# Kernel optimization log

Hardware: AMD Instinct MI355X
Metric: run time of the kernel (lower is better)

The kernel has to match this reference:

```python
import jax, jax.numpy as jnp
import numpy as np

N_NODES = 50000
N_EDGES = 800000
D = 128
BN_EPS = 1e-5


def gcn_conv(x, src, dst, W, b, n_nodes):
    # x: [N, Din]; src/dst: [E+N] (self-loops already appended)
    h = x @ W  # [N, Dout]
    deg = jax.ops.segment_sum(jnp.ones_like(src, dtype=h.dtype), dst, num_segments=n_nodes)
    dinv = jnp.where(deg > 0, jax.lax.rsqrt(deg), 0.0)  # deg^{-1/2}
    norm = dinv[src] * dinv[dst]  # [E+N]
    msg = h[src] * norm[:, None]  # gather + scale
    out = jax.ops.segment_sum(msg, dst, num_segments=n_nodes)  # scatter-add
    return out + b


def batchnorm_prelu(x, gamma, beta, a):
    # training-mode BN over node dim (biased variance), then PReLU
    mu = jnp.mean(x, axis=0)
    var = jnp.mean(jnp.square(x - mu), axis=0)
    xn = (x - mu) * jax.lax.rsqrt(var + BN_EPS)
    y = xn * gamma + beta
    return jnp.where(y >= 0, y, a * y)


def setup_inputs():
    key = jax.random.key(0)
    ks = jax.random.split(key, 8)
    x = jax.random.normal(ks[0], (N_NODES, D), dtype=jnp.float32)
    edge_index = jax.random.randint(ks[1], (2, N_EDGES), 0, N_NODES, dtype=jnp.int32)
    lim = float(np.sqrt(6.0 / (D + D)))  # glorot
    W1 = jax.random.uniform(ks[2], (D, D), jnp.float32, -lim, lim)
    W2 = jax.random.uniform(ks[3], (D, D), jnp.float32, -lim, lim)
    b1 = jnp.zeros((D,), jnp.float32)
    b2 = jnp.zeros((D,), jnp.float32)
    gamma1 = jnp.ones((D,), jnp.float32)
    beta1 = jnp.zeros((D,), jnp.float32)
    gamma2 = jnp.ones((D,), jnp.float32)
    beta2 = jnp.zeros((D,), jnp.float32)
    a1 = jnp.full((1,), 0.25, jnp.float32)
    a2 = jnp.full((1,), 0.25, jnp.float32)
    return {"x": x, "edge_index": edge_index, "W1": W1, "b1": b1, "gamma1": gamma1,
            "beta1": beta1, "a1": a1, "W2": W2, "b2": b2, "gamma2": gamma2,
            "beta2": beta2, "a2": a2}


def reference(x, edge_index, W1, b1, gamma1, beta1, a1, W2, b2, gamma2, beta2, a2):
    n = x.shape[0]
    loops = jnp.arange(n, dtype=edge_index.dtype)
    src = jnp.concatenate([edge_index[0], loops])
    dst = jnp.concatenate([edge_index[1], loops])
    h = gcn_conv(x, src, dst, W1, b1, n)
    h = batchnorm_prelu(h, gamma1, beta1, a1)
    h = gcn_conv(h, src, dst, W2, b2, n)
    h = batchnorm_prelu(h, gamma2, beta2, a2)
    return h
```

## Files before the change

### kernel.cpp

```cpp
#include <hip/hip_runtime.h>
#include <hip/hip_bf16.h>

#define N_NODES 50000
#define N_EDGES 800000
#define D 128
#define BN_EPS 1e-5f
#define GEMM_ROWS 128
#define LDS_PITCH 136

#define BSH 8
#define NB 196
#define TILE 4096
#define NTILES ((N_EDGES + TILE - 1) / TILE)
#define REC_CAP 6144
#define CSR_CHUNKS (REC_CAP / 256)

typedef unsigned short u16;
typedef short bf16x8 __attribute__((ext_vector_type(8)));
typedef float f32x4  __attribute__((ext_vector_type(4)));

__device__ __forceinline__ u16 f2bf(float f) {
    union { float f; unsigned int u; } v; v.f = f;
    unsigned int u = v.u;
    return (u16)((u + 0x7FFF + ((u >> 16) & 1)) >> 16);
}
__device__ __forceinline__ float bflo(unsigned int u) {
    union { unsigned int u; float f; } v; v.u = u << 16; return v.f;
}
__device__ __forceinline__ float bfhi(unsigned int u) {
    union { unsigned int u; float f; } v; v.u = u & 0xFFFF0000u; return v.f;
}
__device__ __forceinline__ unsigned int packbf(float a, float b) {
    return (unsigned int)f2bf(a) | ((unsigned int)f2bf(b) << 16);
}

__global__ __launch_bounds__(256) void hist_prep(const int* __restrict__ dst,
                                                 const float* __restrict__ W1,
                                                 const float* __restrict__ W2,
                                                 int* __restrict__ thist,
                                                 u16* __restrict__ Wt1,
                                                 u16* __restrict__ Wt2,
                                                 float* __restrict__ sums) {
    __shared__ int h[256];
    const int t = threadIdx.x;
    const int b = blockIdx.x;
    if (b < NTILES) {
        h[t] = 0;
        __syncthreads();
        const int e0 = b * TILE;
#pragma unroll
        for (int i = 0; i < 16; ++i) {
            int e = e0 + t + 256 * i;
            if (e < N_EDGES) atomicAdd(&h[dst[e] >> BSH], 1);
        }
        __syncthreads();
        thist[b * 256 + t] = h[t];
    } else {
        const int wb = b - NTILES;
        if (wb == 0) { sums[t] = 0.f; sums[256 + t] = 0.f; }
        int u = wb * 256 + t;
        const float* W = (u < 16384) ? W1 : W2;
        u16* Wt        = (u < 16384) ? Wt1 : Wt2;
        int v = u & 16383;
        int k = v >> 7, n = v & 127;
        Wt[n * 128 + k] = f2bf(W[v]);
    }
}

template <bool BN_IN>
__device__ __forceinline__ void gemm_body(const void* __restrict__ Xv,
                                          const u16* __restrict__ Wt,
                                          u16* __restrict__ C,
                                          const float* __restrict__ sums,
                                          const float* __restrict__ gamma,
                                          const float* __restrict__ beta,
                                          const float* __restrict__ a,
                                          int nrows, int row0,
                                          u16* __restrict__ As,
                                          u16* __restrict__ Ws) {
    const int tid  = threadIdx.x;
    const float invN = 1.0f / (float)N_NODES;

    const bf16x8* Wt8 = (const bf16x8*)Wt;
#pragma unroll
    for (int i = 0; i < 8; ++i) {
        int u = tid + 256 * i;
        int n = u >> 4, kg = u & 15;
        *(bf16x8*)&Ws[n * LDS_PITCH + kg * 8] = Wt8[u];
    }

    if (BN_IN) {
        const uint4* X4 = (const uint4*)Xv;
        const float av = a[0];
#pragma unroll
        for (int i = 0; i < 8; ++i) {
            int u    = tid + 256 * i;
            int r    = u >> 4, kg = u & 15;
            int grow = row0 + r;
            uint4 o = make_uint4(0, 0, 0, 0);
            if (grow < nrows) {
                uint4 v = X4[(size_t)grow * 16 + kg];
                float f[8] = { bflo(v.x), bfhi(v.x), bflo(v.y), bfhi(v.y),
                               bflo(v.z), bfhi(v.z), bflo(v.w), bfhi(v.w) };
#pragma unroll
                for (int c = 0; c < 8; ++c) {
                    int fe     = kg * 8 + c;
                    float mean = sums[fe] * invN;
                    float var  = sums[128 + fe] * invN - mean * mean;
                    float sc   = rsqrtf(var + BN_EPS) * gamma[fe];
                    float y    = (f[c] - mean) * sc + beta[fe];
                    f[c]       = (y >= 0.f) ? y : av * y;
                }
                o.x = packbf(f[0], f[1]); o.y = packbf(f[2], f[3]);
                o.z = packbf(f[4], f[5]); o.w = packbf(f[6], f[7]);
            }
            *(uint4*)&As[r * LDS_PITCH + kg * 8] = o;
        }
    } else {
        const float4* X4 = (const float4*)Xv;
#pragma unroll
        for (int i = 0; i < 16; ++i) {
            int u    = tid + 256 * i;
            int r    = u >> 5, kf = u & 31;
            int grow = row0 + r;
            float4 v = make_float4(0.f, 0.f, 0.f, 0.f);
            if (grow < nrows) v = X4[(size_t)grow * 32 + kf];
            ushort4 p;
            p.x = f2bf(v.x); p.y = f2bf(v.y); p.z = f2bf(v.z); p.w = f2bf(v.w);
            *(ushort4*)&As[r * LDS_PITCH + kf * 4] = p;
        }
    }
    __syncthreads();

    const int wv   = tid >> 6;
    const int lane = tid & 63;
    const int n    = lane & 15;
    const int q    = lane >> 4;
    const int c0   = wv * 32;

    bf16x8 bfr[4][2];
#pragma unroll
    for (int kb = 0; kb < 4; ++kb)
#pragma unroll
        for (int c = 0; c < 2; ++c)
            bfr[kb][c] = *(const bf16x8*)&Ws[(c0 + 16 * c + n) * LDS_PITCH + 32 * kb + 8 * q];

    f32x4 acc[8][2];
    const f32x4 z = {0.f, 0.f, 0.f, 0.f};
#pragma unroll
    for (int rt = 0; rt < 8; ++rt) { acc[rt][0] = z; acc[rt][1] = z; }

#pragma unroll
    for (int kb = 0; kb < 4; ++kb) {
#pragma unroll
        for (int rt = 0; rt < 8; ++rt) {
            bf16x8 af = *(const bf16x8*)&As[(16 * rt + n) * LDS_PITCH + 32 * kb + 8 * q];
            acc[rt][0] = __builtin_amdgcn_mfma_f32_16x16x32_bf16(af, bfr[kb][0], acc[rt][0], 0, 0, 0);
            acc[rt][1] = __builtin_amdgcn_mfma_f32_16x16x32_bf16(af, bfr[kb][1], acc[rt][1], 0, 0, 0);
        }
    }

#pragma unroll
    for (int rt = 0; rt < 8; ++rt) {
        int gr0 = row0 + 16 * rt + 4 * q;
#pragma unroll
        for (int r = 0; r < 4; ++r) {
            int gr = gr0 + r;
            if (gr < nrows) {
                C[(size_t)gr * D + c0 + n]      = f2bf(acc[rt][0][r]);
                C[(size_t)gr * D + c0 + 16 + n] = f2bf(acc[rt][1][r]);
            }
        }
    }
}

__device__ __forceinline__ unsigned long long match8(int key, bool valid) {
    unsigned long long vm = __ballot(valid ? 1 : 0);
    unsigned long long m  = ~0ull;
#pragma unroll
    for (int bit = 0; bit < 8; ++bit) {
        unsigned long long vb = __ballot((key >> bit) & 1);
        m &= ((key >> bit) & 1) ? vb : ~vb;
    }
    return m & vm;
}

__global__ __launch_bounds__(256) void scatter_gemm1(const int* __restrict__ src,
                                                     const int* __restrict__ dst,
                                                     const int* __restrict__ thist,
                                                     unsigned int* __restrict__ brec,
                                                     int* __restrict__ btot,
                                                     int* __restrict__ bbase,
                                                     int* __restrict__ row_ptr,
                                                     const float* __restrict__ x,
                                                     const u16* __restrict__ Wt1,
                                                     u16* __restrict__ C) {
    __shared__ __align__(16) u16 smem[2 * 128 * LDS_PITCH];

    if (blockIdx.x >= NTILES) {
        gemm_body<false>(x, Wt1, C, nullptr, nullptr, nullptr, nullptr,
                         N_NODES, (int)(blockIdx.x - NTILES) * GEMM_ROWS,
                         smem, smem + 128 * LDS_PITCH);
        return;
    }

    int* wcnt  = (int*)smem;
    int* sb    = wcnt + 4 * 256;
    int* lbase = sb + 256;
    int* gbase = lbase + 256;
    unsigned int*  rec = (unsigned int*)(gbase + 256);
    unsigned char* rbk = (unsigned char*)(rec + TILE);

    const int tile = blockIdx.x;
    const int t    = threadIdx.x;
    const int lane = t & 63;
    const int w    = t >> 6;
    const int e0   = tile * TILE;
    const int tcount = min(TILE, N_EDGES - e0);
    const unsigned long long lt = (1ull << lane) - 1ull;

    wcnt[t] = 0; wcnt[256 + t] = 0; wcnt[512 + t] = 0; wcnt[768 + t] = 0;
    __syncthreads();

    unsigned int myrec[16];
    int          myb[16];
    int          myrank[16];
#pragma unroll
    for (int i = 0; i < 16; ++i) {
        int e = e0 + t + 256 * i;
        bool valid = (e < N_EDGES);
        unsigned int s_ = 0, d_ = 0;
        if (valid) { s_ = (unsigned int)src[e]; d_ = (unsigned int)dst[e]; }
        int b = valid ? (int)(d_ >> BSH) : 0;
        myb[i]   = valid ? b : -1;
        myrec[i] = s_ | ((d_ & 255u) << 16);
        unsigned long long m = match8(b, valid);
        int pre  = __popcll(m & lt);
        int base = wcnt[w * 256 + b];
        myrank[i] = base + pre;
        if (valid && pre == 0) wcnt[w * 256 + b] = base + __popcll(m);
    }
    __syncthreads();

    int c0 = wcnt[t], c1 = wcnt[256 + t], c2 = wcnt[512 + t], c3 = wcnt[768 + t];
    int tot_l = c0 + c1 + c2 + c3;
    wcnt[t] = 0; wcnt[256 + t] = c0; wcnt[512 + t] = c0 + c1; wcnt[768 + t] = c0 + c1 + c2;
    sb[t] = tot_l;
    __syncthreads();
#pragma unroll
    for (int off = 1; off < 256; off <<= 1) {
        int add = (t >= off) ? sb[t - off] : 0;
        __syncthreads();
        sb[t] += add;
        __syncthreads();
    }
    lbase[t] = sb[t] - tot_l;
    __syncthreads();

#pragma unroll
    for (int i = 0; i < 16; ++i) {
        if (myb[i] >= 0) {
            int p = lbase[myb[i]] + wcnt[w * 256 + myb[i]] + myrank[i];
            rec[p] = myrec[i];
            rbk[p] = (unsigned char)myb[i];
        }
    }

    int tot = 0, pre = 0;
    for (int j = 0; j < NTILES; ++j) {
        int v = thist[j * 256 + t];
        tot += v;
        if (j < tile) pre += v;
    }
    __syncthreads();
    sb[t] = tot;
    __syncthreads();
#pragma unroll
    for (int off = 1; off < 256; off <<= 1) {
        int add = (t >= off) ? sb[t - off] : 0;
        __syncthreads();
        sb[t] += add;
        __syncthreads();
    }
    int bb = sb[t] - tot;
    gbase[t] = bb + pre;
    if (tile == NTILES - 1 && t < NB) {
        btot[t]  = tot;
        bbase[t] = bb;
        if (t == 0) row_ptr[N_NODES] = N_EDGES;
    }
    __syncthreads();

    for (int i = t; i < tcount; i += 256) {
        int b = rbk[i];
        brec[gbase[b] + (i - lbase[b])] = rec[i];
    }
}

__global__ __launch_bounds__(256) void bucket_csr(const unsigned int* __restrict__ brec,
                                                  const int* __restrict__ bbase,
                                                  const int* __restrict__ btot,
                                                  int* __restrict__ row_ptr,
                                                  u16* __restrict__ col,
                                                  float* __restrict__ dinv) {
    __shared__ unsigned int rec[REC_CAP];
    __shared__ u16 cls[REC_CAP];
    __shared__ int wcnt[4 * 256];
    __shared__ int sb[256];
    __shared__ int lb[256];
    const int b    = blockIdx.x;
    const int t    = threadIdx.x;
    const int lane = t & 63;
    const int w    = t >> 6;
    const int base = bbase[b];
    const int cnt  = min(btot[b], REC_CAP);
    const int n0   = b << BSH;
    const int nn   = min(256, N_NODES - n0);
    const unsigned long long lt = (1ull << lane) - 1ull;

    for (int i = t; i < cnt; i += 256) rec[i] = brec[base + i];
    wcnt[t] = 0; wcnt[256 + t] = 0; wcnt[512 + t] = 0; wcnt[768 + t] = 0;
    __syncthreads();

    int myrank[CSR_CHUNKS];
#pragma unroll
    for (int kk = 0; kk < CSR_CHUNKS; ++kk) {
        int i = t + 256 * kk;
        bool valid = (i < cnt);
        int c = valid ? (int)((rec[i] >> 16) & 255u) : 0;
        unsigned long long m = match8(c, valid);
        int pre  = __popcll(m & lt);
        int bs_  = wcnt[w * 256 + c];
        myrank[kk] = bs_ + pre;
        if (valid && pre == 0) wcnt[w * 256 + c] = bs_ + __popcll(m);
    }
    __syncthreads();

    int c0 = wcnt[t], c1 = wcnt[256 + t], c2 = wcnt[512 + t], c3 = wcnt[768 + t];
    int tot = c0 + c1 + c2 + c3;
    wcnt[t] = 0; wcnt[256 + t] = c0; wcnt[512 + t] = c0 + c1; wcnt[768 + t] = c0 + c1 + c2;
    sb[t] = tot;
    __syncthreads();
#pragma unroll
    for (int off = 1; off < 256; off <<= 1) {
        int add = (t >= off) ? sb[t - off] : 0;
        __syncthreads();
        sb[t] += add;
        __syncthreads();
    }
    int excl = sb[t] - tot;
    lb[t] = excl;
    if (t < nn) {
        row_ptr[n0 + t] = base + excl;
        dinv[n0 + t]    = rsqrtf((float)tot + 1.0f);
    }
    __syncthreads();

#pragma unroll
    for (int kk = 0; kk < CSR_CHUNKS; ++kk) {
        int i = t + 256 * kk;
        if (i < cnt) {
            unsigned int r = rec[i];
            int c = (int)((r >> 16) & 255u);
            int p = lb[c] + wcnt[w * 256 + c] + myrank[kk];
            cls[p] = (u16)(r & 0xFFFFu);
        }
    }
    __syncthreads();
    for (int i = t; i < cnt; i += 256) col[base + i] = cls[i];
}

__global__ __launch_bounds__(256) void gemm2_k(const u16* __restrict__ Obf,
                                               const u16* __restrict__ Wt2,
                                               u16* __restrict__ C,
                                               const float* __restrict__ sums,
                                               const float* __restrict__ gamma,
                                               const float* __restrict__ beta,
                                               const float* __restrict__ a) {
    __shared__ __align__(16) u16 smem[2 * 128 * LDS_PITCH];
    gemm_body<true>(Obf, Wt2, C, sums, gamma, beta, a,
                    N_NODES, (int)blockIdx.x * GEMM_ROWS,
                    smem, smem + 128 * LDS_PITCH);
}

__global__ __launch_bounds__(256, 4) void pull_agg_bn(const u16* __restrict__ H,
                                                      const int* __restrict__ row_ptr,
                                                      const u16* __restrict__ col,
                                                      const float* __restrict__ dinv,
                                                      u16* __restrict__ out,
                                                      float* __restrict__ sums) {
    const int sub  = threadIdx.x & 15;
    const int grp  = (blockIdx.x * blockDim.x + threadIdx.x) >> 4;
    const int ngrp = (gridDim.x * blockDim.x) >> 4;
    const uint4* H4   = (const uint4*)H;
    uint4*       out4 = (uint4*)out;

    float bs[8] = {0.f, 0.f, 0.f, 0.f, 0.f, 0.f, 0.f, 0.f};
    float bq[8] = {0.f, 0.f, 0.f, 0.f, 0.f, 0.f, 0.f, 0.f};

    for (int d = grp; d < N_NODES; d += ngrp) {
        const int beg = row_ptr[d];
        const int end = row_ptr[d + 1];
        const float dv = dinv[d];
        float a0[8], a1[8] = {}, a2[8] = {}, a3[8] = {};
        {
            uint4 v = H4[(size_t)d * 16 + sub];
            a0[0] = dv * bflo(v.x); a0[1] = dv * bfhi(v.x);
            a0[2] = dv * bflo(v.y); a0[3] = dv * bfhi(v.y);
            a0[4] = dv * bflo(v.z); a0[5] = dv * bfhi(v.z);
            a0[6] = dv * bflo(v.w); a0[7] = dv * bfhi(v.w);
        }
        int j = beg;
        for (; j + 3 < end; j += 4) {
            const int s0 = col[j], s1 = col[j + 1], s2 = col[j + 2], s3 = col[j + 3];
            const float d0 = dinv[s0], d1 = dinv[s1], d2 = dinv[s2], d3 = dinv[s3];
            const uint4 v0 = H4[(size_t)s0 * 16 + sub];
            const uint4 v1 = H4[(size_t)s1 * 16 + sub];
            const uint4 v2 = H4[(size_t)s2 * 16 + sub];
            const uint4 v3 = H4[(size_t)s3 * 16 + sub];
            a0[0] += d0 * bflo(v0.x); a0[1] += d0 * bfhi(v0.x);
            a0[2] += d0 * bflo(v0.y); a0[3] += d0 * bfhi(v0.y);
            a0[4] += d0 * bflo(v0.z); a0[5] += d0 * bfhi(v0.z);
            a0[6] += d0 * bflo(v0.w); a0[7] += d0 * bfhi(v0.w);
            a1[0] += d1 * bflo(v1.x); a1[1] += d1 * bfhi(v1.x);
            a1[2] += d1 * bflo(v1.y); a1[3] += d1 * bfhi(v1.y);
            a1[4] += d1 * bflo(v1.z); a1[5] += d1 * bfhi(v1.z);
            a1[6] += d1 * bflo(v1.w); a1[7] += d1 * bfhi(v1.w);
            a2[0] += d2 * bflo(v2.x); a2[1] += d2 * bfhi(v2.x);
            a2[2] += d2 * bflo(v2.y); a2[3] += d2 * bfhi(v2.y);
            a2[4] += d2 * bflo(v2.z); a2[5] += d2 * bfhi(v2.z);
            a2[6] += d2 * bflo(v2.w); a2[7] += d2 * bfhi(v2.w);
            a3[0] += d3 * bflo(v3.x); a3[1] += d3 * bfhi(v3.x);
            a3[2] += d3 * bflo(v3.y); a3[3] += d3 * bfhi(v3.y);
            a3[4] += d3 * bflo(v3.z); a3[5] += d3 * bfhi(v3.z);
            a3[6] += d3 * bflo(v3.w); a3[7] += d3 * bfhi(v3.w);
        }
        for (; j < end; ++j) {
            const int s0 = col[j];
            const float d0 = dinv[s0];
            const uint4 v = H4[(size_t)s0 * 16 + sub];
            a0[0] += d0 * bflo(v.x); a0[1] += d0 * bfhi(v.x);
            a0[2] += d0 * bflo(v.y); a0[3] += d0 * bfhi(v.y);
            a0[4] += d0 * bflo(v.z); a0[5] += d0 * bfhi(v.z);
            a0[6] += d0 * bflo(v.w); a0[7] += d0 * bfhi(v.w);
        }
        float r[8];
#pragma unroll
        for (int c = 0; c < 8; ++c) r[c] = ((a0[c] + a1[c]) + (a2[c] + a3[c])) * dv;
        uint4 o;
        o.x = packbf(r[0], r[1]); o.y = packbf(r[2], r[3]);
        o.z = packbf(r[4], r[5]); o.w = packbf(r[6], r[7]);
        out4[(size_t)d * 16 + sub] = o;

#pragma unroll
        for (int c = 0; c < 8; ++c) { bs[c] += r[c]; bq[c] += r[c] * r[c]; }
    }

#pragma unroll
    for (int c = 0; c < 8; ++c) {
        bs[c] += __shfl_xor(bs[c], 16, 64);
        bs[c] += __shfl_xor(bs[c], 32, 64);
        bq[c] += __shfl_xor(bq[c], 16, 64);
        bq[c] += __shfl_xor(bq[c], 32, 64);
    }

    __shared__ float ls[4 * 256];
    const int lane = threadIdx.x & 63;
    const int wv   = threadIdx.x >> 6;
    if (lane < 16) {
#pragma unroll
        for (int c = 0; c < 8; ++c) {
            ls[wv * 256 + lane * 16 + c]     = bs[c];
            ls[wv * 256 + lane * 16 + 8 + c] = bq[c];
        }
    }
    __syncthreads();

    const int s2 = threadIdx.x >> 4;
    const int vi = threadIdx.x & 15;
    float v = ((ls[s2 * 16 + vi] + ls[256 + s2 * 16 + vi]) +
               (ls[512 + s2 * 16 + vi] + ls[768 + s2 * 16 + vi]));
    const int f = s2 * 8 + (vi & 7);
    atomicAdd(&sums[(vi < 8) ? f : (128 + f)], v);
}

__global__ void bn_prelu_bf(const u16* __restrict__ X, const float* __restrict__ sums,
                            const float* __restrict__ gamma, const float* __restrict__ beta,
                            const float* __restrict__ a, float* __restrict__ out,
                            float invN) {
    int idx = blockIdx.x * blockDim.x + threadIdx.x;
    if (idx >= N_NODES * 64) return;
    unsigned int u = ((const unsigned int*)X)[idx];
    int f0 = (idx * 2) & 127;
    float av = a[0];
    float2 o;
    {
        float mean = sums[f0] * invN;
        float var  = sums[128 + f0] * invN - mean * mean;
        float sc   = rsqrtf(var + BN_EPS) * gamma[f0];
        float y    = (bflo(u) - mean) * sc + beta[f0];
        o.x = (y >= 0.f) ? y : av * y;
    }
    {
        int f1 = f0 + 1;
        float mean = sums[f1] * invN;
        float var  = sums[128 + f1] * invN - mean * mean;
        float sc   = rsqrtf(var + BN_EPS) * gamma[f1];
        float y    = (bfhi(u) - mean) * sc + beta[f1];
        o.y = (y >= 0.f) ? y : av * y;
    }
    ((float2*)out)[idx] = o;
}

extern "C" void kernel_launch(void* const* d_in, const int* in_sizes, int n_in,
                              void* d_out, int out_size, void* d_ws, size_t ws_size,
                              hipStream_t stream) {
    const float* x      = (const float*)d_in[0];
    const int*   edges  = (const int*)d_in[1];
    const float* W1     = (const float*)d_in[2];
    const float* gamma1 = (const float*)d_in[4];
    const float* beta1  = (const float*)d_in[5];
    const float* a1     = (const float*)d_in[6];
    const float* W2     = (const float*)d_in[7];
    const float* gamma2 = (const float*)d_in[9];
    const float* beta2  = (const float*)d_in[10];
    const float* a2     = (const float*)d_in[11];

    const int* src = edges;
    const int* dst = edges + N_EDGES;

    float* OUT = (float*)d_out;
    char* ws = (char*)d_ws;
    u16*   Abf      = (u16*)ws;    ws += (size_t)N_NODES * D * sizeof(u16);
    u16*   Obf      = (u16*)ws;    ws += (size_t)N_NODES * D * sizeof(u16);
    float* dinv     = (float*)ws;  ws += N_NODES * sizeof(float);
    float* sums     = (float*)ws;  ws += 512 * sizeof(float);
    int*   row_ptr  = (int*)ws;    ws += (N_NODES + 1) * sizeof(int);
    int*   btot     = (int*)ws;    ws += NB * sizeof(int);
    int*   bbase    = (int*)ws;    ws += NB * sizeof(int);
    int*   thist    = (int*)ws;    ws += (size_t)NTILES * 256 * sizeof(int);
    unsigned int* brec = (unsigned int*)ws; ws += (size_t)N_EDGES * sizeof(unsigned int);
    u16*   col      = (u16*)ws;    ws += (size_t)N_EDGES * sizeof(u16);
    u16*   Wt1      = (u16*)ws;    ws += 16384 * sizeof(u16);
    u16*   Wt2      = (u16*)ws;    ws += 16384 * sizeof(u16);

    const float invN = 1.0f / (float)N_NODES;
    const int gemmGrid = (N_NODES + GEMM_ROWS - 1) / GEMM_ROWS;
    const int prGrid   = (N_NODES * 64 + 255) / 256;

    hist_prep<<<NTILES + 128, 256, 0, stream>>>(dst, W1, W2, thist, Wt1, Wt2, sums);

    scatter_gemm1<<<NTILES + gemmGrid, 256, 0, stream>>>(src, dst, thist, brec,
                                                         btot, bbase, row_ptr,
                                                         x, Wt1, Abf);
    bucket_csr<<<NB, 256, 0, stream>>>(brec, bbase, btot, row_ptr, col, dinv);

    pull_agg_bn<<<2048, 256, 0, stream>>>(Abf, row_ptr, col, dinv, Obf, sums);

    gemm2_k<<<gemmGrid, 256, 0, stream>>>(Obf, Wt2, Abf, sums, gamma1, beta1, a1);
    pull_agg_bn<<<2048, 256, 0, stream>>>(Abf, row_ptr, col, dinv, Obf, sums + 256);
    bn_prelu_bf<<<prGrid, 256, 0, stream>>>(Obf, sums + 256, gamma2, beta2, a2, OUT, invN);
}
```

Baseline: 299.7 us.

## Launch one 16-lane group per node and batch eight neighbor gathers per iteration

Replaces the grid-stride loop in the pull aggregation kernel with one 16-thread group per destination node, launching exactly N_NODES*16 threads. The neighbor loop now issues eight col/dinv/H gathers at once, with clamped indices and zeroed weights for the tail, so more loads are in flight. The aim is more memory-level parallelism and less loop overhead. In exchange it launches far more blocks, each doing its own BN-stat reduction and atomics, and wastes gathers on padded tail slots.

```diff
diff --git a/kernel.cpp b/kernel.cpp
--- a/kernel.cpp
+++ b/kernel.cpp
@@ -389,73 +389,62 @@
                                                       const float* __restrict__ dinv,
                                                       u16* __restrict__ out,
                                                       float* __restrict__ sums) {
-    const int sub  = threadIdx.x & 15;
-    const int grp  = (blockIdx.x * blockDim.x + threadIdx.x) >> 4;
-    const int ngrp = (gridDim.x * blockDim.x) >> 4;
+    const int sub = threadIdx.x & 15;
+    const int d   = (blockIdx.x * 256 + threadIdx.x) >> 4;
     const uint4* H4   = (const uint4*)H;
     uint4*       out4 = (uint4*)out;
 
-    float bs[8] = {0.f, 0.f, 0.f, 0.f, 0.f, 0.f, 0.f, 0.f};
-    float bq[8] = {0.f, 0.f, 0.f, 0.f, 0.f, 0.f, 0.f, 0.f};
-
-    for (int d = grp; d < N_NODES; d += ngrp) {
-        const int beg = row_ptr[d];
-        const int end = row_ptr[d + 1];
-        const float dv = dinv[d];
-        float a0[8], a1[8] = {}, a2[8] = {}, a3[8] = {};
-        {
-            uint4 v = H4[(size_t)d * 16 + sub];
-            a0[0] = dv * bflo(v.x); a0[1] = dv * bfhi(v.x);
-            a0[2] = dv * bflo(v.y); a0[3] = dv * bfhi(v.y);
-            a0[4] = dv * bflo(v.z); a0[5] = dv * bfhi(v.z);
-            a0[6] = dv * bflo(v.w); a0[7] = dv * bfhi(v.w);
-        }
-        int j = beg;
-        for (; j + 3 < end; j += 4) {
-            const int s0 = col[j], s1 = col[j + 1], s2 = col[j + 2], s3 = col[j + 3];
-            const float d0 = dinv[s0], d1 = dinv[s1], d2 = dinv[s2], d3 = dinv[s3];
-            const uint4 v0 = H4[(size_t)s0 * 16 + sub];
-            const uint4 v1 = H4[(size_t)s1 * 16 + sub];
-            const uint4 v2 = H4[(size_t)s2 * 16 + sub];
-            const uint4 v3 = H4[(size_t)s3 * 16 + sub];
-            a0[0] += d0 * bflo(v0.x); a0[1] += d0 * bfhi(v0.x);
-            a0[2] += d0 * bflo(v0.y); a0[3] += d0 * bfhi(v0.y);
-            a0[4] += d0 * bflo(v0.z); a0[5] += d0 * bfhi(v0.z);
-            a0[6] += d0 * bflo(v0.w); a0[7] += d0 * bfhi(v0.w);
-            a1[0] += d1 * bflo(v1.x); a1[1] += d1 * bfhi(v1.x);
-            a1[2] += d1 * bflo(v1.y); a1[3] += d1 * bfhi(v1.y);
-            a1[4] += d1 * bflo(v1.z); a1[5] += d1 * bfhi(v1.z);
-            a1[6] += d1 * bflo(v1.w); a1[7] += d1 * bfhi(v1.w);
-            a2[0] += d2 * bflo(v2.x); a2[1] += d2 * bfhi(v2.x);
-            a2[2] += d2 * bflo(v2.y); a2[3] += d2 * bfhi(v2.y);
-            a2[4] += d2 * bflo(v2.z); a2[5] += d2 * bfhi(v2.z);
-            a2[6] += d2 * bflo(v2.w); a2[7] += d2 * bfhi(v2.w);
-            a3[0] += d3 * bflo(v3.x); a3[1] += d3 * bfhi(v3.x);
-            a3[2] += d3 * bflo(v3.y); a3[3] += d3 * bfhi(v3.y);
-            a3[4] += d3 * bflo(v3.z); a3[5] += d3 * bfhi(v3.z);
-            a3[6] += d3 * bflo(v3.w); a3[7] += d3 * bfhi(v3.w);
-        }
-        for (; j < end; ++j) {
-            const int s0 = col[j];
-            const float d0 = dinv[s0];
-            const uint4 v = H4[(size_t)s0 * 16 + sub];
-            a0[0] += d0 * bflo(v.x); a0[1] += d0 * bfhi(v.x);
-            a0[2] += d0 * bflo(v.y); a0[3] += d0 * bfhi(v.y);
-            a0[4] += d0 * bflo(v.z); a0[5] += d0 * bfhi(v.z);
-            a0[6] += d0 * bflo(v.w); a0[7] += d0 * bfhi(v.w);
-        }
-        float r[8];
-#pragma unroll
-        for (int c = 0; c < 8; ++c) r[c] = ((a0[c] + a1[c]) + (a2[c] + a3[c])) * dv;
-        uint4 o;
-        o.x = packbf(r[0], r[1]); o.y = packbf(r[2], r[3]);
-        o.z = packbf(r[4], r[5]); o.w = packbf(r[6], r[7]);
-        out4[(size_t)d * 16 + sub] = o;
-
-#pragma unroll
-        for (int c = 0; c < 8; ++c) { bs[c] += r[c]; bq[c] += r[c] * r[c]; }
-    }
-
+    const int beg = row_ptr[d];
+    const int end = row_ptr[d + 1];
+    const float dv = dinv[d];
+    float a0[8], a1[8] = {};
+    {
+        uint4 v = H4[(size_t)d * 16 + sub];
+        a0[0] = dv * bflo(v.x); a0[1] = dv * bfhi(v.x);
+        a0[2] = dv * bflo(v.y); a0[3] = dv * bfhi(v.y);
+        a0[4] = dv * bflo(v.z); a0[5] = dv * bfhi(v.z);
+        a0[6] = dv * bflo(v.w); a0[7] = dv * bfhi(v.w);
+    }
+    for (int j = beg; j < end; j += 8) {
+        int   s[8];
+        float dd[8];
+        uint4 w[8];
+#pragma unroll
+        for (int k = 0; k < 8; ++k) {
+            int jj = j + k;
+            int jc = (jj < end) ? jj : (end - 1);
+            s[k] = (int)col[jc];
+        }
+#pragma unroll
+        for (int k = 0; k < 8; ++k) {
+            float dk = dinv[s[k]];
+            dd[k] = (j + k < end) ? dk : 0.f;
+        }
+#pragma unroll
+        for (int k = 0; k < 8; ++k) w[k] = H4[(size_t)s[k] * 16 + sub];
+#pragma unroll
+        for (int k = 0; k < 8; k += 2) {
+            a0[0] += dd[k] * bflo(w[k].x); a0[1] += dd[k] * bfhi(w[k].x);
+            a0[2] += dd[k] * bflo(w[k].y); a0[3] += dd[k] * bfhi(w[k].y);
+            a0[4] += dd[k] * bflo(w[k].z); a0[5] += dd[k] * bfhi(w[k].z);
+            a0[6] += dd[k] * bflo(w[k].w); a0[7] += dd[k] * bfhi(w[k].w);
+            a1[0] += dd[k + 1] * bflo(w[k + 1].x); a1[1] += dd[k + 1] * bfhi(w[k + 1].x);
+            a1[2] += dd[k + 1] * bflo(w[k + 1].y); a1[3] += dd[k + 1] * bfhi(w[k + 1].y);
+            a1[4] += dd[k + 1] * bflo(w[k + 1].z); a1[5] += dd[k + 1] * bfhi(w[k + 1].z);
+            a1[6] += dd[k + 1] * bflo(w[k + 1].w); a1[7] += dd[k + 1] * bfhi(w[k + 1].w);
+        }
+    }
+    float r[8];
+#pragma unroll
+    for (int c = 0; c < 8; ++c) r[c] = (a0[c] + a1[c]) * dv;
+    uint4 o;
+    o.x = packbf(r[0], r[1]); o.y = packbf(r[2], r[3]);
+    o.z = packbf(r[4], r[5]); o.w = packbf(r[6], r[7]);
+    out4[(size_t)d * 16 + sub] = o;
+
+    float bs[8], bq[8];
+#pragma unroll
+    for (int c = 0; c < 8; ++c) { bs[c] = r[c]; bq[c] = r[c] * r[c]; }
 #pragma unroll
     for (int c = 0; c < 8; ++c) {
         bs[c] += __shfl_xor(bs[c], 16, 64);
@@ -546,6 +535,7 @@
 
     const float invN = 1.0f / (float)N_NODES;
     const int gemmGrid = (N_NODES + GEMM_ROWS - 1) / GEMM_ROWS;
+    const int pullGrid = (N_NODES * 16) / 256;
     const int prGrid   = (N_NODES * 64 + 255) / 256;
 
     hist_prep<<<NTILES + 128, 256, 0, stream>>>(dst, W1, W2, thist, Wt1, Wt2, sums);
@@ -555,9 +545,9 @@
                                                          x, Wt1, Abf);
     bucket_csr<<<NB, 256, 0, stream>>>(brec, bbase, btot, row_ptr, col, dinv);
 
-    pull_agg_bn<<<2048, 256, 0, stream>>>(Abf, row_ptr, col, dinv, Obf, sums);
+    pull_agg_bn<<<pullGrid, 256, 0, stream>>>(Abf, row_ptr, col, dinv, Obf, sums);
 
     gemm2_k<<<gemmGrid, 256, 0, stream>>>(Obf, Wt2, Abf, sums, gamma1, beta1, a1);
-    pull_agg_bn<<<2048, 256, 0, stream>>>(Abf, row_ptr, col, dinv, Obf, sums + 256);
+    pull_agg_bn<<<pullGrid, 256, 0, stream>>>(Abf, row_ptr, col, dinv, Obf, sums + 256);
     bn_prelu_bf<<<prGrid, 256, 0, stream>>>(Obf, sums + 256, gamma2, beta2, a2, OUT, invN);
 }
```

Measured after the change: 344.3 us. 1.15x slower.

## Prescale node features by dinv before aggregation to drop per-edge dinv gathers

Applied to the files above, without the earlier changes.

Moves the source-side deg^{-1/2} scaling out of the edge loop. Layer 1 features are rescaled in place inside bucket_csr once dinv is known, and layer 2 GEMM output is scaled in its epilogue. The pull aggregation then only sums gathered rows and multiplies by the destination dinv. This removes one random dinv load and a multiply per edge, at the cost of an extra read-modify-write pass over the layer-1 feature matrix and one more bf16 rounding step.

```diff
diff --git a/kernel.cpp b/kernel.cpp
--- a/kernel.cpp
+++ b/kernel.cpp
@@ -67,7 +67,7 @@
     }
 }
 
-template <bool BN_IN>
+template <bool BN_IN, bool SCALE>
 __device__ __forceinline__ void gemm_body(const void* __restrict__ Xv,
                                           const u16* __restrict__ Wt,
                                           u16* __restrict__ C,
@@ -75,6 +75,7 @@
                                           const float* __restrict__ gamma,
                                           const float* __restrict__ beta,
                                           const float* __restrict__ a,
+                                          const float* __restrict__ dinv,
                                           int nrows, int row0,
                                           u16* __restrict__ As,
                                           u16* __restrict__ Ws) {
@@ -167,8 +168,9 @@
         for (int r = 0; r < 4; ++r) {
             int gr = gr0 + r;
             if (gr < nrows) {
-                C[(size_t)gr * D + c0 + n]      = f2bf(acc[rt][0][r]);
-                C[(size_t)gr * D + c0 + 16 + n] = f2bf(acc[rt][1][r]);
+                float dv = SCALE ? dinv[gr] : 1.0f;
+                C[(size_t)gr * D + c0 + n]      = f2bf(acc[rt][0][r] * dv);
+                C[(size_t)gr * D + c0 + 16 + n] = f2bf(acc[rt][1][r] * dv);
             }
         }
     }
@@ -198,9 +200,9 @@
     __shared__ __align__(16) u16 smem[2 * 128 * LDS_PITCH];
 
     if (blockIdx.x >= NTILES) {
-        gemm_body<false>(x, Wt1, C, nullptr, nullptr, nullptr, nullptr,
-                         N_NODES, (int)(blockIdx.x - NTILES) * GEMM_ROWS,
-                         smem, smem + 128 * LDS_PITCH);
+        gemm_body<false, false>(x, Wt1, C, nullptr, nullptr, nullptr, nullptr, nullptr,
+                                N_NODES, (int)(blockIdx.x - NTILES) * GEMM_ROWS,
+                                smem, smem + 128 * LDS_PITCH);
         return;
     }
 
@@ -302,12 +304,14 @@
                                                   const int* __restrict__ btot,
                                                   int* __restrict__ row_ptr,
                                                   u16* __restrict__ col,
-                                                  float* __restrict__ dinv) {
+                                                  float* __restrict__ dinv,
+                                                  u16* __restrict__ Abf) {
     __shared__ unsigned int rec[REC_CAP];
     __shared__ u16 cls[REC_CAP];
     __shared__ int wcnt[4 * 256];
     __shared__ int sb[256];
     __shared__ int lb[256];
+    __shared__ float dvs[256];
     const int b    = blockIdx.x;
     const int t    = threadIdx.x;
     const int lane = t & 63;
@@ -340,6 +344,8 @@
     int tot = c0 + c1 + c2 + c3;
     wcnt[t] = 0; wcnt[256 + t] = c0; wcnt[512 + t] = c0 + c1; wcnt[768 + t] = c0 + c1 + c2;
     sb[t] = tot;
+    float dvt = rsqrtf((float)tot + 1.0f);
+    dvs[t] = dvt;
     __syncthreads();
 #pragma unroll
     for (int off = 1; off < 256; off <<= 1) {
@@ -352,7 +358,7 @@
     lb[t] = excl;
     if (t < nn) {
         row_ptr[n0 + t] = base + excl;
-        dinv[n0 + t]    = rsqrtf((float)tot + 1.0f);
+        dinv[n0 + t]    = dvt;
     }
     __syncthreads();
 
@@ -368,6 +374,14 @@
     }
     __syncthreads();
     for (int i = t; i < cnt; i += 256) col[base + i] = cls[i];
+
+    unsigned int* A32 = (unsigned int*)(Abf + (size_t)n0 * D);
+    const int nu = nn * 64;
+    for (int i = t; i < nu; i += 256) {
+        float dv = dvs[i >> 6];
+        unsigned int u = A32[i];
+        A32[i] = packbf(dv * bflo(u), dv * bfhi(u));
+    }
 }
 
 __global__ __launch_bounds__(256) void gemm2_k(const u16* __restrict__ Obf,
@@ -376,11 +390,12 @@
                                                const float* __restrict__ sums,
                                                const float* __restrict__ gamma,
                                                const float* __restrict__ beta,
-                                               const float* __restrict__ a) {
+                                               const float* __restrict__ a,
+                                               const float* __restrict__ dinv) {
     __shared__ __align__(16) u16 smem[2 * 128 * LDS_PITCH];
-    gemm_body<true>(Obf, Wt2, C, sums, gamma, beta, a,
-                    N_NODES, (int)blockIdx.x * GEMM_ROWS,
-                    smem, smem + 128 * LDS_PITCH);
+    gemm_body<true, true>(Obf, Wt2, C, sums, gamma, beta, a, dinv,
+                          N_NODES, (int)blockIdx.x * GEMM_ROWS,
+                          smem, smem + 128 * LDS_PITCH);
 }
 
 __global__ __launch_bounds__(256, 4) void pull_agg_bn(const u16* __restrict__ H,
@@ -401,49 +416,34 @@
     for (int d = grp; d < N_NODES; d += ngrp) {
         const int beg = row_ptr[d];
         const int end = row_ptr[d + 1];
-        const float dv = dinv[d];
         float a0[8], a1[8] = {}, a2[8] = {}, a3[8] = {};
         {
             uint4 v = H4[(size_t)d * 16 + sub];
-            a0[0] = dv * bflo(v.x); a0[1] = dv * bfhi(v.x);
-            a0[2] = dv * bflo(v.y); a0[3] = dv * bfhi(v.y);
-            a0[4] = dv * bflo(v.z); a0[5] = dv * bfhi(v.z);
-            a0[6] = dv * bflo(v.w); a0[7] = dv * bfhi(v.w);
+            a0[0] = bflo(v.x); a0[1] = bfhi(v.x); a0[2] = bflo(v.y); a0[3] = bfhi(v.y);
+            a0[4] = bflo(v.z); a0[5] = bfhi(v.z); a0[6] = bflo(v.w); a0[7] = bfhi(v.w);
         }
         int j = beg;
         for (; j + 3 < end; j += 4) {
             const int s0 = col[j], s1 = col[j + 1], s2 = col[j + 2], s3 = col[j + 3];
-            const float d0 = dinv[s0], d1 = dinv[s1], d2 = dinv[s2], d3 = dinv[s3];
             const uint4 v0 = H4[(size_t)s0 * 16 + sub];
             const uint4 v1 = H4[(size_t)s1 * 16 + sub];
             const uint4 v2 = H4[(size_t)s2 * 16 + sub];
             const uint4 v3 = H4[(size_t)s3 * 16 + sub];
-            a0[0] += d0 * bflo(v0.x); a0[1] += d0 * bfhi(v0.x);
-            a0[2] += d0 * bflo(v0.y); a0[3] += d0 * bfhi(v0.y);
-            a0[4] += d0 * bflo(v0.z); a0[5] += d0 * bfhi(v0.z);
-            a0[6] += d0 * bflo(v0.w); a0[7] += d0 * bfhi(v0.w);
-            a1[0] += d1 * bflo(v1.x); a1[1] += d1 * bfhi(v1.x);
-            a1[2] += d1 * bflo(v1.y); a1[3] += d1 * bfhi(v1.y);
-            a1[4] += d1 * bflo(v1.z); a1[5] += d1 * bfhi(v1.z);
-            a1[6] += d1 * bflo(v1.w); a1[7] += d1 * bfhi(v1.w);
-            a2[0] += d2 * bflo(v2.x); a2[1] += d2 * bfhi(v2.x);
-            a2[2] += d2 * bflo(v2.y); a2[3] += d2 * bfhi(v2.y);
-            a2[4] += d2 * bflo(v2.z); a2[5] += d2 * bfhi(v2.z);
-            a2[6] += d2 * bflo(v2.w); a2[7] += d2 * bfhi(v2.w);
-            a3[0] += d3 * bflo(v3.x); a3[1] += d3 * bfhi(v3.x);
-            a3[2] += d3 * bflo(v3.y); a3[3] += d3 * bfhi(v3.y);
-            a3[4] += d3 * bflo(v3.z); a3[5] += d3 * bfhi(v3.z);
-            a3[6] += d3 * bflo(v3.w); a3[7] += d3 * bfhi(v3.w);
+            a0[0] += bflo(v0.x); a0[1] += bfhi(v0.x); a0[2] += bflo(v0.y); a0[3] += bfhi(v0.y);
+            a0[4] += bflo(v0.z); a0[5] += bfhi(v0.z); a0[6] += bflo(v0.w); a0[7] += bfhi(v0.w);
+            a1[0] += bflo(v1.x); a1[1] += bfhi(v1.x); a1[2] += bflo(v1.y); a1[3] += bfhi(v1.y);
+            a1[4] += bflo(v1.z); a1[5] += bfhi(v1.z); a1[6] += bflo(v1.w); a1[7] += bfhi(v1.w);
+            a2[0] += bflo(v2.x); a2[1] += bfhi(v2.x); a2[2] += bflo(v2.y); a2[3] += bfhi(v2.y);
+            a2[4] += bflo(v2.z); a2[5] += bfhi(v2.z); a2[6] += bflo(v2.w); a2[7] += bfhi(v2.w);
+            a3[0] += bflo(v3.x); a3[1] += bfhi(v3.x); a3[2] += bflo(v3.y); a3[3] += bfhi(v3.y);
+            a3[4] += bflo(v3.z); a3[5] += bfhi(v3.z); a3[6] += bflo(v3.w); a3[7] += bfhi(v3.w);
         }
         for (; j < end; ++j) {
-            const int s0 = col[j];
-            const float d0 = dinv[s0];
-            const uint4 v = H4[(size_t)s0 * 16 + sub];
-            a0[0] += d0 * bflo(v.x); a0[1] += d0 * bfhi(v.x);
-            a0[2] += d0 * bflo(v.y); a0[3] += d0 * bfhi(v.y);
-            a0[4] += d0 * bflo(v.z); a0[5] += d0 * bfhi(v.z);
-            a0[6] += d0 * bflo(v.w); a0[7] += d0 * bfhi(v.w);
-        }
+            const uint4 v = H4[(size_t)col[j] * 16 + sub];
+            a0[0] += bflo(v.x); a0[1] += bfhi(v.x); a0[2] += bflo(v.y); a0[3] += bfhi(v.y);
+            a0[4] += bflo(v.z); a0[5] += bfhi(v.z); a0[6] += bflo(v.w); a0[7] += bfhi(v.w);
+        }
+        const float dv = dinv[d];
         float r[8];
 #pragma unroll
         for (int c = 0; c < 8; ++c) r[c] = ((a0[c] + a1[c]) + (a2[c] + a3[c])) * dv;
@@ -546,6 +546,7 @@
 
     const float invN = 1.0f / (float)N_NODES;
     const int gemmGrid = (N_NODES + GEMM_ROWS - 1) / GEMM_ROWS;
+    const int pullGrid = 2048;
     const int prGrid   = (N_NODES * 64 + 255) / 256;
 
     hist_prep<<<NTILES + 128, 256, 0, stream>>>(dst, W1, W2, thist, Wt1, Wt2, sums);
@@ -553,11 +554,11 @@
     scatter_gemm1<<<NTILES + gemmGrid, 256, 0, stream>>>(src, dst, thist, brec,
                                                          btot, bbase, row_ptr,
                                                          x, Wt1, Abf);
-    bucket_csr<<<NB, 256, 0, stream>>>(brec, bbase, btot, row_ptr, col, dinv);
-
-    pull_agg_bn<<<2048, 256, 0, stream>>>(Abf, row_ptr, col, dinv, Obf, sums);
-
-    gemm2_k<<<gemmGrid, 256, 0, stream>>>(Obf, Wt2, Abf, sums, gamma1, beta1, a1);
-    pull_agg_bn<<<2048, 256, 0, stream>>>(Abf, row_ptr, col, dinv, Obf, sums + 256);
+    bucket_csr<<<NB, 256, 0, stream>>>(brec, bbase, btot, row_ptr, col, dinv, Abf);
+
+    pull_agg_bn<<<pullGrid, 256, 0, stream>>>(Abf, row_ptr, col, dinv, Obf, sums);
+
+    gemm2_k<<<gemmGrid, 256, 0, stream>>>(Obf, Wt2, Abf, sums, gamma1, beta1, a1, dinv);
+    pull_agg_bn<<<pullGrid, 256, 0, stream>>>(Abf, row_ptr, col, dinv, Obf, sums + 256);
     bn_prelu_bf<<<prGrid, 256, 0, stream>>>(Obf, sums + 256, gamma2, beta2, a2, OUT, invN);
 }
```

New measurement: 311.2 us. +3.9%, slower.
